# Optimization experiments

Hardware: AMD Instinct MI355X
Metric: run time of the kernel (lower is better)

## Reference

```python
import jax, jax.numpy as jnp
import numpy as np
import math

EMB = 1024
H = 8          # num_heads
HD = EMB // H // 2  # head_dim = 64
LAMBDA_INIT = 0.8
B, N = 2, 2048


def setup_inputs() -> dict:
    key = jax.random.key(0)
    ks = jax.random.split(key, 16)
    s = 1.0 / math.sqrt(EMB)
    d = {
        'q': jax.random.normal(ks[0], (B, N, EMB), jnp.float32),
        'k': jax.random.normal(ks[1], (B, N, EMB), jnp.float32),
        'v': jax.random.normal(ks[2], (B, N, EMB), jnp.float32),
        'Wq': jax.random.uniform(ks[3], (EMB, EMB), jnp.float32, -s, s),
        'bq': jax.random.uniform(ks[4], (EMB,), jnp.float32, -s, s),
        'Wk': jax.random.uniform(ks[5], (EMB, EMB), jnp.float32, -s, s),
        'bk': jax.random.uniform(ks[6], (EMB,), jnp.float32, -s, s),
        'Wv': jax.random.uniform(ks[7], (EMB, EMB), jnp.float32, -s, s),
        'bv': jax.random.uniform(ks[8], (EMB,), jnp.float32, -s, s),
        'Wo': jax.random.uniform(ks[9], (EMB, EMB), jnp.float32, -s, s),
        'bo': jax.random.uniform(ks[10], (EMB,), jnp.float32, -s, s),
        'lambda_q1': 0.1 * jax.random.normal(ks[11], (HD,), jnp.float32),
        'lambda_k1': 0.1 * jax.random.normal(ks[12], (HD,), jnp.float32),
        'lambda_q2': 0.1 * jax.random.normal(ks[13], (HD,), jnp.float32),
        'lambda_k2': 0.1 * jax.random.normal(ks[14], (HD,), jnp.float32),
    }
    return d


def reference(q, k, v, Wq, bq, Wk, bk, Wv, bv, Wo, bo,
              lambda_q1, lambda_k1, lambda_q2, lambda_k2):
    b, n, _ = q.shape
    # projections (torch Linear: x @ W.T + b)
    qp = q @ Wq.T + bq            # [b, n, EMB]
    kp = k @ Wk.T + bk
    vp = v @ Wv.T + bv
    # split into 2*H sub-heads of width HD for q/k; H heads of width 2*HD for v
    qh = qp.reshape(b, n, 2 * H, HD).transpose(0, 2, 1, 3)   # [b, 2H, n, HD]
    kh = kp.reshape(b, n, 2 * H, HD).transpose(0, 2, 1, 3)   # [b, 2H, n, HD]
    vh = vp.reshape(b, n, H, 2 * HD).transpose(0, 2, 1, 3)   # [b, H, n, 2HD]
    scale = 1.0 / math.sqrt(HD)
    attn = jnp.einsum('bhqd,bhkd->bhqk', qh, kh) * scale      # [b, 2H, n, n]
    attn = jax.nn.softmax(attn, axis=-1)
    lam1 = jnp.exp(jnp.sum(lambda_q1 * lambda_k1))
    lam2 = jnp.exp(jnp.sum(lambda_q2 * lambda_k2))
    lam = lam1 - lam2 + LAMBDA_INIT
    attn = attn.reshape(b, H, 2, n, n)
    diff = attn[:, :, 0] - lam * attn[:, :, 1]                # [b, H, n, n]
    out = jnp.einsum('bhqk,bhkd->bhqd', diff, vh)             # [b, H, n, 2HD]
    out = out.transpose(0, 2, 1, 3).reshape(b, n, H * 2 * HD)
    return out @ Wo.T + bo
```

## Files before the change

### kernel.cpp

```cpp
#include <hip/hip_runtime.h>
#include <stdint.h>


typedef __attribute__((ext_vector_type(8))) __bf16 bf16x8;
typedef __attribute__((ext_vector_type(4))) float f32x4;
typedef __attribute__((ext_vector_type(8))) unsigned short u16x8;
typedef __attribute__((ext_vector_type(4))) unsigned short u16x4;
typedef unsigned short u16;
typedef unsigned int u32;

#define EMB 1024
#define NSEQ 2048
#define NBATCH 2
#define NHEAD 8
#define MROWS (NBATCH*NSEQ)

__device__ __forceinline__ u16 f2bf(float f){
  u32 x = __builtin_bit_cast(u32, f);
  return (u16)((x + 0x7fffu + ((x >> 16) & 1u)) >> 16);
}

__device__ __forceinline__ bf16x8 ld8(const u16* p){
  return __builtin_bit_cast(bf16x8, *(const u16x8*)p);
}

__device__ __forceinline__ void glds16(const u16* g, u16* l){
  __builtin_amdgcn_global_load_lds(
      (const __attribute__((address_space(1))) u32*)g,
      (__attribute__((address_space(3))) u32*)l, 16, 0, 0);
}

__global__ void cvt_k(const float* __restrict__ q, const float* __restrict__ k,
                      const float* __restrict__ v, const float* __restrict__ Wq,
                      const float* __restrict__ Wk, const float* __restrict__ Wv,
                      const float* __restrict__ Wo,
                      u16* qb, u16* kb, u16* vb, u16* Wqb, u16* Wkb, u16* Wvb, u16* Wob)
{
  const int NQ4 = (NBATCH*NSEQ*EMB)/4;
  const int NW4 = (EMB*EMB)/4;
  const int total = 3*NQ4 + 4*NW4;
  for (int i = blockIdx.x*blockDim.x + threadIdx.x; i < total; i += gridDim.x*blockDim.x){
    const float* src; u16* dst; int off;
    if (i < 3*NQ4){
      int t = i / NQ4; off = i - t*NQ4;
      src = t==0 ? q : (t==1 ? k : v);
      dst = t==0 ? qb : (t==1 ? kb : vb);
    } else {
      int j = i - 3*NQ4;
      int t = j / NW4; off = j - t*NW4;
      src = t==0 ? Wq : (t==1 ? Wk : (t==2 ? Wv : Wo));
      dst = t==0 ? Wqb : (t==1 ? Wkb : (t==2 ? Wvb : Wob));
    }
    f32x4 f = *((const f32x4*)src + off);
    u16x4 u; u[0]=f2bf(f[0]); u[1]=f2bf(f[1]); u[2]=f2bf(f[2]); u[3]=f2bf(f[3]);
    *((u16x4*)dst + off) = u;
  }
}

__global__ void lambda_k(const float* __restrict__ lq1, const float* __restrict__ lk1,
                         const float* __restrict__ lq2, const float* __restrict__ lk2,
                         float* lam)
{
  int l = threadIdx.x;
  float p1 = lq1[l]*lk1[l];
  float p2 = lq2[l]*lk2[l];
  #pragma unroll
  for (int m=1; m<64; m<<=1){ p1 += __shfl_xor(p1, m, 64); p2 += __shfl_xor(p2, m, 64); }
  if (l==0) lam[0] = __expf(p1) - __expf(p2) + 0.8f;
}

__device__ __forceinline__ void gemm_core(
    const u16* __restrict__ A, const u16* __restrict__ W, const float* __restrict__ bias,
    u16* __restrict__ Ybf, u16* __restrict__ Yvt, float* __restrict__ Yf, int mode,
    u16* As, u16* Bs)
{
  const int tid = threadIdx.x, w = tid >> 6, l = tid & 63;
  const int l15 = l & 15, lg = l >> 4;
  const int m0 = blockIdx.y * 128, n0 = blockIdx.x * 128;
  const int wr = w >> 1, wc = w & 1;
  const int srow = w*16 + (l >> 2);
  const int skel = (l & 3) * 8;

  f32x4 acc[4][4] = {};

  for (int kt = 0; kt < EMB/32; ++kt){
    const int kb = kt*32 + skel;
    glds16(A + (size_t)(m0 + srow)*EMB + kb,      As + w*512);
    glds16(A + (size_t)(m0 + 64 + srow)*EMB + kb, As + 2048 + w*512);
    glds16(W + (size_t)(n0 + srow)*EMB + kb,      Bs + w*512);
    glds16(W + (size_t)(n0 + 64 + srow)*EMB + kb, Bs + 2048 + w*512);
    __syncthreads();

    bf16x8 af[4], bfr[4];
    #pragma unroll
    for (int mi=0; mi<4; ++mi) af[mi]  = ld8(As + (wr*64 + mi*16 + l15)*32 + lg*8);
    #pragma unroll
    for (int ni=0; ni<4; ++ni) bfr[ni] = ld8(Bs + (wc*64 + ni*16 + l15)*32 + lg*8);
    #pragma unroll
    for (int mi=0; mi<4; ++mi)
      #pragma unroll
      for (int ni=0; ni<4; ++ni)
        acc[mi][ni] = __builtin_amdgcn_mfma_f32_16x16x32_bf16(af[mi], bfr[ni], acc[mi][ni], 0,0,0);
    __syncthreads();
  }

  #pragma unroll
  for (int mi=0; mi<4; ++mi){
    const int mr = m0 + wr*64 + mi*16 + lg*4;
    #pragma unroll
    for (int ni=0; ni<4; ++ni){
      const int nc = n0 + wc*64 + ni*16 + l15;
      const float bv = bias[nc];
      if (mode == 0){
        #pragma unroll
        for (int i=0;i<4;++i) Ybf[(size_t)(mr+i)*EMB + nc] = f2bf(acc[mi][ni][i] + bv);
      } else if (mode == 1){
        const int h = nc >> 7, vd = nc & 127, bb = mr >> 11, t = mr & 2047;
        u16x4 pk;
        #pragma unroll
        for (int i=0;i<4;++i) pk[i] = f2bf(acc[mi][ni][i] + bv);
        *(u16x4*)(Yvt + ((size_t)((bb*NHEAD + h)*128 + vd))*NSEQ + t) = pk;
      } else {
        #pragma unroll
        for (int i=0;i<4;++i) Yf[(size_t)(mr+i)*EMB + nc] = acc[mi][ni][i] + bv;
      }
    }
  }
}

__global__ __launch_bounds__(256) void gemm_qkv(
    const u16* qb, const u16* kb, const u16* vb,
    const u16* Wqb, const u16* Wkb, const u16* Wvb,
    const float* bq, const float* bk, const float* bv,
    u16* Qp, u16* Kp, u16* Vt)
{
  __shared__ __align__(16) u16 As[4096], Bs[4096];
  const int z = blockIdx.z;
  const u16* A = z==0 ? qb : (z==1 ? kb : vb);
  const u16* W = z==0 ? Wqb : (z==1 ? Wkb : Wvb);
  const float* bias = z==0 ? bq : (z==1 ? bk : bv);
  if (z < 2) gemm_core(A, W, bias, z==0 ? Qp : Kp, nullptr, nullptr, 0, As, Bs);
  else       gemm_core(A, W, bias, nullptr, Vt, nullptr, 1, As, Bs);
}

__global__ __launch_bounds__(256) void gemm_out_k(
    const u16* Xc, const u16* Wob, const float* bo, float* out)
{
  __shared__ __align__(16) u16 As[4096], Bs[4096];
  gemm_core(Xc, Wob, bo, nullptr, nullptr, out, 2, As, Bs);
}

__global__ __launch_bounds__(256, 2) void attn_k(
    const u16* __restrict__ Qp, const u16* __restrict__ Kp,
    const u16* __restrict__ Vt, const float* __restrict__ lamp,
    u16* __restrict__ Xc)
{
  __shared__ __align__(16) u16 ldsK[2*64*128];
  __shared__ __align__(16) u16 ldsV[2*128*64];
  __shared__ __align__(16) u16 ldsP[4*2*16*64];

  const int tid = threadIdx.x, w = tid >> 6, l = tid & 63;
  const int l15 = l & 15, lg = l >> 4, rx = l15 & 7;
  int bid = blockIdx.x;
  bid = (bid & 7)*64 + (bid >> 3);
  const int qt = bid & 31, bh = bid >> 5;
  const int b = bh >> 3, h = bh & 7;
  const int q0 = qt*64 + w*16;
  const float C = 0.125f * 1.4426950408889634f;
  const float lam = lamp[0];

  const u16* Kg = Kp + ((size_t)b*NSEQ)*EMB + h*128;
  const u16* Vg = Vt + ((size_t)((b*NHEAD + h)*128))*NSEQ;

  const u16* qbase = Qp + (size_t)(b*NSEQ + q0 + l15)*EMB + 2*h*64;
  bf16x8 qa[2][2];
  #pragma unroll
  for (int s2=0; s2<2; ++s2)
    #pragma unroll
    for (int ks=0; ks<2; ++ks)
      qa[s2][ks] = ld8(qbase + s2*64 + ks*32 + lg*8);

  f32x4 acc[2][8] = {};
  float m_run[2] = {-1e30f, -1e30f}, l_run[2] = {0.f, 0.f};

  u16* Pw = ldsP + w*2048;

  const int srK = l >> 4, ssK = l & 15;
  const int srV = l >> 3, ssV = l & 7;

  auto STAGE = [&](int cur, int kt){
    const u16* kg = Kg + ((size_t)kt*64)*EMB;
    u16* kd = ldsK + cur*8192;
    #pragma unroll
    for (int j=0;j<4;++j){
      int row = w*16 + j*4 + srK;
      glds16(kg + (size_t)row*EMB + ((ssK ^ (row&7))*8), kd + (w*16 + j*4)*128);
    }
    const u16* vg = Vg + kt*64;
    u16* vd2 = ldsV + cur*8192;
    #pragma unroll
    for (int j=0;j<4;++j){
      int row = w*32 + j*8 + srV;
      glds16(vg + (size_t)row*NSEQ + ((ssV ^ (row&7))*8), vd2 + (w*32 + j*8)*64);
    }
  };

  STAGE(0, 0);
  __syncthreads();
  int cur = 0;

  for (int kt = 0; kt < NSEQ/64; ++kt){
    if (kt+1 < NSEQ/64) STAGE(cur^1, kt+1);

    const u16* Kb = ldsK + cur*8192;
    const u16* Vb = ldsV + cur*8192;

    f32x4 st[2][4] = {};
    #pragma unroll
    for (int s2=0; s2<2; ++s2)
      #pragma unroll
      for (int nt=0; nt<4; ++nt)
        #pragma unroll
        for (int ks=0; ks<2; ++ks){
          bf16x8 kf = ld8(Kb + (nt*16 + l15)*128 + (((s2*8 + ks*4 + lg) ^ rx)*8));
          st[s2][nt] = __builtin_amdgcn_mfma_f32_16x16x32_bf16(kf, qa[s2][ks], st[s2][nt], 0,0,0);
        }

    #pragma unroll
    for (int s2=0; s2<2; ++s2){
      float tm = fmaxf(fmaxf(st[s2][0][0], st[s2][0][1]), fmaxf(st[s2][0][2], st[s2][0][3]));
      #pragma unroll
      for (int nt=1; nt<4; ++nt)
        tm = fmaxf(tm, fmaxf(fmaxf(st[s2][nt][0], st[s2][nt][1]),
                             fmaxf(st[s2][nt][2], st[s2][nt][3])));
      tm = fmaxf(tm, __shfl_xor(tm, 16, 64));
      tm = fmaxf(tm, __shfl_xor(tm, 32, 64));
      if (!__all(tm <= m_run[s2] + 8.f)){
        float mn = fmaxf(m_run[s2], tm);
        float al = exp2f((m_run[s2] - mn)*C);
        m_run[s2] = mn;
        l_run[s2] *= al;
        #pragma unroll
        for (int vt=0; vt<8; ++vt){
          acc[s2][vt][0]*=al; acc[s2][vt][1]*=al; acc[s2][vt][2]*=al; acc[s2][vt][3]*=al;
        }
      }
      float ssum = 0.f;
      #pragma unroll
      for (int nt=0; nt<4; ++nt)
        #pragma unroll
        for (int i=0;i<4;++i){
          float pv = exp2f((st[s2][nt][i] - m_run[s2])*C);
          st[s2][nt][i] = pv; ssum += pv;
        }
      ssum += __shfl_xor(ssum, 16, 64);
      ssum += __shfl_xor(ssum, 32, 64);
      l_run[s2] += ssum;

      #pragma unroll
      for (int nt=0; nt<4; ++nt){
        u16x4 pk;
        pk[0]=f2bf(st[s2][nt][0]); pk[1]=f2bf(st[s2][nt][1]);
        pk[2]=f2bf(st[s2][nt][2]); pk[3]=f2bf(st[s2][nt][3]);
        int chunk = 2*nt + (lg>>1);
        *(u16x4*)(Pw + s2*1024 + l15*64 + ((chunk^rx)*8) + (lg&1)*4) = pk;
      }
    }

    bf16x8 pa[2][2];
    #pragma unroll
    for (int s2=0; s2<2; ++s2)
      #pragma unroll
      for (int ks=0; ks<2; ++ks)
        pa[s2][ks] = ld8(Pw + s2*1024 + l15*64 + (((ks*4 + lg)^rx)*8));

    #pragma unroll
    for (int ks=0; ks<2; ++ks)
      #pragma unroll
      for (int vt=0; vt<8; ++vt){
        bf16x8 vf = ld8(Vb + (vt*16 + l15)*64 + (((ks*4 + lg)^rx)*8));
        acc[0][vt] = __builtin_amdgcn_mfma_f32_16x16x32_bf16(vf, pa[0][ks], acc[0][vt], 0,0,0);
        acc[1][vt] = __builtin_amdgcn_mfma_f32_16x16x32_bf16(vf, pa[1][ks], acc[1][vt], 0,0,0);
      }

    __syncthreads();
    cur ^= 1;
  }

  const float i0 = 1.f / l_run[0];
  const float i1 = lam / l_run[1];
  #pragma unroll
  for (int vt=0; vt<8; ++vt){
    u16x4 o;
    #pragma unroll
    for (int i=0;i<4;++i) o[i] = f2bf(acc[0][vt][i]*i0 - acc[1][vt][i]*i1);
    *(u16x4*)(Xc + (size_t)(b*NSEQ + q0 + l15)*EMB + h*128 + vt*16 + lg*4) = o;
  }
}

extern "C" void kernel_launch(void* const* d_in, const int* in_sizes, int n_in,
                              void* d_out, int out_size, void* d_ws, size_t ws_size,
                              hipStream_t stream)
{
  const float* q   = (const float*)d_in[0];
  const float* k   = (const float*)d_in[1];
  const float* v   = (const float*)d_in[2];
  const float* Wq  = (const float*)d_in[3];
  const float* bq  = (const float*)d_in[4];
  const float* Wk  = (const float*)d_in[5];
  const float* bk  = (const float*)d_in[6];
  const float* Wv  = (const float*)d_in[7];
  const float* bv  = (const float*)d_in[8];
  const float* Wo  = (const float*)d_in[9];
  const float* bo  = (const float*)d_in[10];
  const float* lq1 = (const float*)d_in[11];
  const float* lk1 = (const float*)d_in[12];
  const float* lq2 = (const float*)d_in[13];
  const float* lk2 = (const float*)d_in[14];

  const size_t NQ = (size_t)MROWS*EMB;
  const size_t NW = (size_t)EMB*EMB;
  u16* qb  = (u16*)d_ws;
  u16* kb  = qb + NQ;
  u16* vb  = kb + NQ;
  u16* Wqb = vb + NQ;
  u16* Wkb = Wqb + NW;
  u16* Wvb = Wkb + NW;
  u16* Wob = Wvb + NW;
  u16* Qp  = Wob + NW;
  u16* Kp  = Qp + NQ;
  u16* Vt  = Kp + NQ;
  u16* Xc  = Vt + NQ;
  float* lam = (float*)(Xc + NQ);

  cvt_k<<<2048, 256, 0, stream>>>(q, k, v, Wq, Wk, Wv, Wo,
                                  qb, kb, vb, Wqb, Wkb, Wvb, Wob);
  lambda_k<<<1, 64, 0, stream>>>(lq1, lk1, lq2, lk2, lam);
  gemm_qkv<<<dim3(EMB/128, MROWS/128, 3), 256, 0, stream>>>(
      qb, kb, vb, Wqb, Wkb, Wvb, bq, bk, bv, Qp, Kp, Vt);
  attn_k<<<dim3(NBATCH*NHEAD*(NSEQ/64)), 256, 0, stream>>>(Qp, Kp, Vt, lam, Xc);
  gemm_out_k<<<dim3(EMB/128, MROWS/128), 256, 0, stream>>>(Xc, Wob, bo, (float*)d_out);
}
```

Measured before the change: 181.8 us.

## Shrink attention KV tile, fold softmax scale into Q, use native bf16 conversion

```diff
diff --git a/kernel.cpp b/kernel.cpp
--- a/kernel.cpp
+++ b/kernel.cpp
@@ -3,6 +3,7 @@
 
 
 typedef __attribute__((ext_vector_type(8))) __bf16 bf16x8;
+typedef __attribute__((ext_vector_type(4))) __bf16 bf16x4;
 typedef __attribute__((ext_vector_type(4))) float f32x4;
 typedef __attribute__((ext_vector_type(8))) unsigned short u16x8;
 typedef __attribute__((ext_vector_type(4))) unsigned short u16x4;
@@ -14,10 +15,14 @@
 #define NBATCH 2
 #define NHEAD 8
 #define MROWS (NBATCH*NSEQ)
-
-__device__ __forceinline__ u16 f2bf(float f){
-  u32 x = __builtin_bit_cast(u32, f);
-  return (u16)((x + 0x7fffu + ((x >> 16) & 1u)) >> 16);
+#define QSCALE 0.18033688011112042f
+
+__device__ __forceinline__ u16x4 pk4(float a, float b, float c, float d){
+  bf16x4 h; h[0]=(__bf16)a; h[1]=(__bf16)b; h[2]=(__bf16)c; h[3]=(__bf16)d;
+  return __builtin_bit_cast(u16x4, h);
+}
+__device__ __forceinline__ u16 bf1(float f){
+  __bf16 h = (__bf16)f; return __builtin_bit_cast(unsigned short, h);
 }
 
 __device__ __forceinline__ bf16x8 ld8(const u16* p){
@@ -52,8 +57,7 @@
       dst = t==0 ? Wqb : (t==1 ? Wkb : (t==2 ? Wvb : Wob));
     }
     f32x4 f = *((const f32x4*)src + off);
-    u16x4 u; u[0]=f2bf(f[0]); u[1]=f2bf(f[1]); u[2]=f2bf(f[2]); u[3]=f2bf(f[3]);
-    *((u16x4*)dst + off) = u;
+    *((u16x4*)dst + off) = pk4(f[0], f[1], f[2], f[3]);
   }
 }
 
@@ -72,7 +76,7 @@
 __device__ __forceinline__ void gemm_core(
     const u16* __restrict__ A, const u16* __restrict__ W, const float* __restrict__ bias,
     u16* __restrict__ Ybf, u16* __restrict__ Yvt, float* __restrict__ Yf, int mode,
-    u16* As, u16* Bs)
+    float oscale, u16* As, u16* Bs)
 {
   const int tid = threadIdx.x, w = tid >> 6, l = tid & 63;
   const int l15 = l & 15, lg = l >> 4;
@@ -110,19 +114,18 @@
     #pragma unroll
     for (int ni=0; ni<4; ++ni){
       const int nc = n0 + wc*64 + ni*16 + l15;
-      const float bv = bias[nc];
+      const float bvs = bias[nc]*oscale;
       if (mode == 0){
         #pragma unroll
-        for (int i=0;i<4;++i) Ybf[(size_t)(mr+i)*EMB + nc] = f2bf(acc[mi][ni][i] + bv);
+        for (int i=0;i<4;++i) Ybf[(size_t)(mr+i)*EMB + nc] = bf1(fmaf(acc[mi][ni][i], oscale, bvs));
       } else if (mode == 1){
         const int h = nc >> 7, vd = nc & 127, bb = mr >> 11, t = mr & 2047;
-        u16x4 pk;
-        #pragma unroll
-        for (int i=0;i<4;++i) pk[i] = f2bf(acc[mi][ni][i] + bv);
-        *(u16x4*)(Yvt + ((size_t)((bb*NHEAD + h)*128 + vd))*NSEQ + t) = pk;
+        u16x4 pkv = pk4(acc[mi][ni][0]+bvs, acc[mi][ni][1]+bvs,
+                        acc[mi][ni][2]+bvs, acc[mi][ni][3]+bvs);
+        *(u16x4*)(Yvt + ((size_t)((bb*NHEAD + h)*128 + vd))*NSEQ + t) = pkv;
       } else {
         #pragma unroll
-        for (int i=0;i<4;++i) Yf[(size_t)(mr+i)*EMB + nc] = acc[mi][ni][i] + bv;
+        for (int i=0;i<4;++i) Yf[(size_t)(mr+i)*EMB + nc] = acc[mi][ni][i] + bvs;
       }
     }
   }
@@ -139,34 +142,35 @@
   const u16* A = z==0 ? qb : (z==1 ? kb : vb);
   const u16* W = z==0 ? Wqb : (z==1 ? Wkb : Wvb);
   const float* bias = z==0 ? bq : (z==1 ? bk : bv);
-  if (z < 2) gemm_core(A, W, bias, z==0 ? Qp : Kp, nullptr, nullptr, 0, As, Bs);
-  else       gemm_core(A, W, bias, nullptr, Vt, nullptr, 1, As, Bs);
+  if (z == 0)      gemm_core(A, W, bias, Qp, nullptr, nullptr, 0, QSCALE, As, Bs);
+  else if (z == 1) gemm_core(A, W, bias, Kp, nullptr, nullptr, 0, 1.0f, As, Bs);
+  else             gemm_core(A, W, bias, nullptr, Vt, nullptr, 1, 1.0f, As, Bs);
 }
 
 __global__ __launch_bounds__(256) void gemm_out_k(
     const u16* Xc, const u16* Wob, const float* bo, float* out)
 {
   __shared__ __align__(16) u16 As[4096], Bs[4096];
-  gemm_core(Xc, Wob, bo, nullptr, nullptr, out, 2, As, Bs);
-}
-
-__global__ __launch_bounds__(256, 2) void attn_k(
+  gemm_core(Xc, Wob, bo, nullptr, nullptr, out, 2, 1.0f, As, Bs);
+}
+
+__global__ __launch_bounds__(256, 4) void attn_k(
     const u16* __restrict__ Qp, const u16* __restrict__ Kp,
     const u16* __restrict__ Vt, const float* __restrict__ lamp,
     u16* __restrict__ Xc)
 {
-  __shared__ __align__(16) u16 ldsK[2*64*128];
-  __shared__ __align__(16) u16 ldsV[2*128*64];
-  __shared__ __align__(16) u16 ldsP[4*2*16*64];
+  __shared__ __align__(16) u16 ldsK[2*32*128];
+  __shared__ __align__(16) u16 ldsV[2*128*32];
+  __shared__ __align__(16) u16 ldsP[4*2*16*32];
 
   const int tid = threadIdx.x, w = tid >> 6, l = tid & 63;
-  const int l15 = l & 15, lg = l >> 4, rx = l15 & 7;
+  const int l15 = l & 15, lg = l >> 4;
+  const int rx7 = l15 & 7, rx3 = l15 & 3;
   int bid = blockIdx.x;
   bid = (bid & 7)*64 + (bid >> 3);
   const int qt = bid & 31, bh = bid >> 5;
   const int b = bh >> 3, h = bh & 7;
   const int q0 = qt*64 + w*16;
-  const float C = 0.125f * 1.4426950408889634f;
   const float lam = lamp[0];
 
   const u16* Kg = Kp + ((size_t)b*NSEQ)*EMB + h*128;
@@ -183,25 +187,22 @@
   f32x4 acc[2][8] = {};
   float m_run[2] = {-1e30f, -1e30f}, l_run[2] = {0.f, 0.f};
 
-  u16* Pw = ldsP + w*2048;
-
-  const int srK = l >> 4, ssK = l & 15;
-  const int srV = l >> 3, ssV = l & 7;
+  u16* Pw = ldsP + w*1024;
 
   auto STAGE = [&](int cur, int kt){
-    const u16* kg = Kg + ((size_t)kt*64)*EMB;
-    u16* kd = ldsK + cur*8192;
-    #pragma unroll
-    for (int j=0;j<4;++j){
-      int row = w*16 + j*4 + srK;
-      glds16(kg + (size_t)row*EMB + ((ssK ^ (row&7))*8), kd + (w*16 + j*4)*128);
-    }
-    const u16* vg = Vg + kt*64;
-    u16* vd2 = ldsV + cur*8192;
-    #pragma unroll
-    for (int j=0;j<4;++j){
-      int row = w*32 + j*8 + srV;
-      glds16(vg + (size_t)row*NSEQ + ((ssV ^ (row&7))*8), vd2 + (w*32 + j*8)*64);
+    const u16* kg = Kg + ((size_t)kt*32)*EMB;
+    u16* kd = ldsK + cur*4096;
+    #pragma unroll
+    for (int j=0;j<2;++j){
+      int row = w*8 + j*4 + (l >> 4);
+      glds16(kg + (size_t)row*EMB + (((l&15) ^ (row&7))*8), kd + (w*8 + j*4)*128);
+    }
+    const u16* vg = Vg + kt*32;
+    u16* vd2 = ldsV + cur*4096;
+    #pragma unroll
+    for (int j=0;j<2;++j){
+      int row = w*32 + j*16 + (l >> 2);
+      glds16(vg + (size_t)row*NSEQ + (((l&3) ^ (row&3))*8), vd2 + (w*32 + j*16)*32);
     }
   };
 
@@ -209,35 +210,34 @@
   __syncthreads();
   int cur = 0;
 
-  for (int kt = 0; kt < NSEQ/64; ++kt){
-    if (kt+1 < NSEQ/64) STAGE(cur^1, kt+1);
-
-    const u16* Kb = ldsK + cur*8192;
-    const u16* Vb = ldsV + cur*8192;
-
-    f32x4 st[2][4] = {};
+  for (int kt = 0; kt < NSEQ/32; ++kt){
+    if (kt+1 < NSEQ/32) STAGE(cur^1, kt+1);
+
+    const u16* Kb = ldsK + cur*4096;
+    const u16* Vb = ldsV + cur*4096;
+
+    f32x4 st[2][2] = {};
+    __builtin_amdgcn_s_setprio(1);
     #pragma unroll
     for (int s2=0; s2<2; ++s2)
       #pragma unroll
-      for (int nt=0; nt<4; ++nt)
+      for (int nt=0; nt<2; ++nt)
         #pragma unroll
         for (int ks=0; ks<2; ++ks){
-          bf16x8 kf = ld8(Kb + (nt*16 + l15)*128 + (((s2*8 + ks*4 + lg) ^ rx)*8));
+          bf16x8 kf = ld8(Kb + (nt*16 + l15)*128 + (((s2*8 + ks*4 + lg) ^ rx7)*8));
           st[s2][nt] = __builtin_amdgcn_mfma_f32_16x16x32_bf16(kf, qa[s2][ks], st[s2][nt], 0,0,0);
         }
+    __builtin_amdgcn_s_setprio(0);
 
     #pragma unroll
     for (int s2=0; s2<2; ++s2){
       float tm = fmaxf(fmaxf(st[s2][0][0], st[s2][0][1]), fmaxf(st[s2][0][2], st[s2][0][3]));
-      #pragma unroll
-      for (int nt=1; nt<4; ++nt)
-        tm = fmaxf(tm, fmaxf(fmaxf(st[s2][nt][0], st[s2][nt][1]),
-                             fmaxf(st[s2][nt][2], st[s2][nt][3])));
+      tm = fmaxf(tm, fmaxf(fmaxf(st[s2][1][0], st[s2][1][1]), fmaxf(st[s2][1][2], st[s2][1][3])));
       tm = fmaxf(tm, __shfl_xor(tm, 16, 64));
       tm = fmaxf(tm, __shfl_xor(tm, 32, 64));
-      if (!__all(tm <= m_run[s2] + 8.f)){
+      if (!__all(tm <= m_run[s2] + 11.5f)){
         float mn = fmaxf(m_run[s2], tm);
-        float al = exp2f((m_run[s2] - mn)*C);
+        float al = exp2f(m_run[s2] - mn);
         m_run[s2] = mn;
         l_run[s2] *= al;
         #pragma unroll
@@ -247,10 +247,10 @@
       }
       float ssum = 0.f;
       #pragma unroll
-      for (int nt=0; nt<4; ++nt)
+      for (int nt=0; nt<2; ++nt)
         #pragma unroll
         for (int i=0;i<4;++i){
-          float pv = exp2f((st[s2][nt][i] - m_run[s2])*C);
+          float pv = exp2f(st[s2][nt][i] - m_run[s2]);
           st[s2][nt][i] = pv; ssum += pv;
         }
       ssum += __shfl_xor(ssum, 16, 64);
@@ -258,30 +258,23 @@
       l_run[s2] += ssum;
 
       #pragma unroll
-      for (int nt=0; nt<4; ++nt){
-        u16x4 pk;
-        pk[0]=f2bf(st[s2][nt][0]); pk[1]=f2bf(st[s2][nt][1]);
-        pk[2]=f2bf(st[s2][nt][2]); pk[3]=f2bf(st[s2][nt][3]);
-        int chunk = 2*nt + (lg>>1);
-        *(u16x4*)(Pw + s2*1024 + l15*64 + ((chunk^rx)*8) + (lg&1)*4) = pk;
+      for (int nt=0; nt<2; ++nt){
+        u16x4 pkv = pk4(st[s2][nt][0], st[s2][nt][1], st[s2][nt][2], st[s2][nt][3]);
+        *(u16x4*)(Pw + s2*512 + l15*32 + (((nt*2 + (lg>>1)) ^ rx3)*8) + (lg&1)*4) = pkv;
       }
     }
 
-    bf16x8 pa[2][2];
-    #pragma unroll
-    for (int s2=0; s2<2; ++s2)
-      #pragma unroll
-      for (int ks=0; ks<2; ++ks)
-        pa[s2][ks] = ld8(Pw + s2*1024 + l15*64 + (((ks*4 + lg)^rx)*8));
-
-    #pragma unroll
-    for (int ks=0; ks<2; ++ks)
-      #pragma unroll
-      for (int vt=0; vt<8; ++vt){
-        bf16x8 vf = ld8(Vb + (vt*16 + l15)*64 + (((ks*4 + lg)^rx)*8));
-        acc[0][vt] = __builtin_amdgcn_mfma_f32_16x16x32_bf16(vf, pa[0][ks], acc[0][vt], 0,0,0);
-        acc[1][vt] = __builtin_amdgcn_mfma_f32_16x16x32_bf16(vf, pa[1][ks], acc[1][vt], 0,0,0);
-      }
+    bf16x8 pa0 = ld8(Pw +       l15*32 + ((lg ^ rx3)*8));
+    bf16x8 pa1 = ld8(Pw + 512 + l15*32 + ((lg ^ rx3)*8));
+
+    __builtin_amdgcn_s_setprio(1);
+    #pragma unroll
+    for (int vt=0; vt<8; ++vt){
+      bf16x8 vf = ld8(Vb + (vt*16 + l15)*32 + ((lg ^ rx3)*8));
+      acc[0][vt] = __builtin_amdgcn_mfma_f32_16x16x32_bf16(vf, pa0, acc[0][vt], 0,0,0);
+      acc[1][vt] = __builtin_amdgcn_mfma_f32_16x16x32_bf16(vf, pa1, acc[1][vt], 0,0,0);
+    }
+    __builtin_amdgcn_s_setprio(0);
 
     __syncthreads();
     cur ^= 1;
@@ -291,9 +284,10 @@
   const float i1 = lam / l_run[1];
   #pragma unroll
   for (int vt=0; vt<8; ++vt){
-    u16x4 o;
-    #pragma unroll
-    for (int i=0;i<4;++i) o[i] = f2bf(acc[0][vt][i]*i0 - acc[1][vt][i]*i1);
+    u16x4 o = pk4(acc[0][vt][0]*i0 - acc[1][vt][0]*i1,
+                  acc[0][vt][1]*i0 - acc[1][vt][1]*i1,
+                  acc[0][vt][2]*i0 - acc[1][vt][2]*i1,
+                  acc[0][vt][3]*i0 - acc[1][vt][3]*i1);
     *(u16x4*)(Xc + (size_t)(b*NSEQ + q0 + l15)*EMB + h*128 + vt*16 + lg*4) = o;
   }
 }
```

After: 221.1 us. +21.7%, slower.
